# Optimization experiments

Hardware: AMD Instinct MI355X
Metric: run time of the kernel (lower is better)

Reference implementation:

```python
import jax, jax.numpy as jnp
import numpy as np

B, S, D, H = 2, 2048, 1024, 16  # batch, seq, embed_dim, num_heads
DH = D // H                      # head dim = 64


def setup_inputs() -> dict:
    key = jax.random.key(0)
    kx, kq, kbq, kk, kbk, kv, kbv = jax.random.split(key, 7)
    scale = 1.0 / np.sqrt(D)
    return {
        "x": jax.random.normal(kx, (B, S, D), dtype=jnp.float32),
        "Wq": jax.random.normal(kq, (D, D), dtype=jnp.float32) * scale,
        "bq": jax.random.normal(kbq, (D,), dtype=jnp.float32) * 0.01,
        "Wk": jax.random.normal(kk, (D, D), dtype=jnp.float32) * scale,
        "bk": jax.random.normal(kbk, (D,), dtype=jnp.float32) * 0.01,
        "Wv": jax.random.normal(kv, (D, D), dtype=jnp.float32) * scale,
        "bv": jax.random.normal(kbv, (D,), dtype=jnp.float32) * 0.01,
    }


def reference(x, Wq, bq, Wk, bk, Wv, bv):
    # ooqkv_type == 'q', odeint_method == 'id': q branch = act(Linear(x)), exact GELU (torch nn.GELU default)
    q = jax.nn.gelu(x @ Wq + bq, approximate=False)
    k = x @ Wk + bk
    v = x @ Wv + bv
    # [B, S, D] -> [B, S, H, DH]
    q = q.reshape(B, S, H, DH)
    k = k.reshape(B, S, H, DH)
    v = v.reshape(B, S, H, DH)
    # NOTE: original module has NO 1/sqrt(d) scale — faithful reproduction
    att = jnp.einsum("bqhd,bkhd->bhqk", q, k)
    att = jax.nn.softmax(att, axis=-1)
    out = jnp.einsum("bhqk,bkhd->bqhd", att, v)
    return out.reshape(B, S, D)
```

## Files before the change

### kernel.cpp

```cpp
#include <hip/hip_runtime.h>
#include <math.h>

#define B_  2
#define S_  2048
#define D_  1024
#define H_  16
#define DH_ 64
#define M_  (B_ * S_)

typedef _Float16 half_t;
typedef __attribute__((ext_vector_type(8))) _Float16 h8;
typedef __attribute__((ext_vector_type(4))) _Float16 h4;
typedef __attribute__((ext_vector_type(4))) float   f32x4;

__device__ __forceinline__ void gll16(const half_t* g, half_t* l) {
    __builtin_amdgcn_global_load_lds(
        (__attribute__((address_space(1))) const void*)g,
        (__attribute__((address_space(3))) void*)l, 16, 0, 0);
}

__global__ __launch_bounds__(256) void convert_x_k(
    const float* __restrict__ x, half_t* __restrict__ xh)
{
    const size_t i = ((size_t)blockIdx.x * 256 + threadIdx.x) * 8;
    const float4 a = *(const float4*)(x + i);
    const float4 b = *(const float4*)(x + i + 4);
    h8 o;
    o[0] = (half_t)a.x; o[1] = (half_t)a.y; o[2] = (half_t)a.z; o[3] = (half_t)a.w;
    o[4] = (half_t)b.x; o[5] = (half_t)b.y; o[6] = (half_t)b.z; o[7] = (half_t)b.w;
    *(h8*)(xh + i) = o;
}

__global__ __launch_bounds__(256) void transW_k(
    const float* __restrict__ Wq, const float* __restrict__ Wk,
    const float* __restrict__ Wv, half_t* __restrict__ Wt)
{
    const int which = blockIdx.y;
    const float* __restrict__ W = (which == 0) ? Wq : (which == 1) ? Wk : Wv;
    half_t* __restrict__ T = Wt + (size_t)which * D_ * D_;
    const int gw   = blockIdx.x * 4 + (threadIdx.x >> 6);
    const int lane = threadIdx.x & 63;
    const int n    = (gw & 15) * 64 + lane;
    const int k0   = (gw >> 4) * 8;
    h8 o;
    #pragma unroll
    for (int t = 0; t < 8; ++t) o[t] = (half_t)W[(size_t)(k0 + t) * D_ + n];
    *(h8*)(T + (size_t)n * D_ + k0) = o;
}

__global__ __launch_bounds__(256) void transV_k(
    const half_t* __restrict__ V, half_t* __restrict__ Vt)
{
    const int gw   = blockIdx.x * 4 + (threadIdx.x >> 6);
    const int lane = threadIdx.x & 63;
    const int bh   = gw >> 8;
    const int s0   = (gw & 255) * 8;
    const int b    = bh >> 4, h = bh & 15;
    h8 o;
    #pragma unroll
    for (int t = 0; t < 8; ++t)
        o[t] = V[((size_t)b * S_ + s0 + t) * D_ + h * DH_ + lane];
    *(h8*)(Vt + ((size_t)bh * DH_ + lane) * S_ + s0) = o;
}

__global__ __launch_bounds__(256) void qkv_gemm_f16(
    const half_t* __restrict__ xh, const half_t* __restrict__ Wt,
    const float* __restrict__ bq, const float* __restrict__ bk,
    const float* __restrict__ bv,
    half_t* __restrict__ Qo, half_t* __restrict__ Ko, half_t* __restrict__ Vo)
{
    const int n0g   = blockIdx.x * 128;
    const int which = n0g >> 10;
    const int n0    = n0g & 1023;
    const int m0    = blockIdx.y * 128;
    const half_t* __restrict__ Wp  = Wt + (size_t)which * D_ * D_;
    const float* __restrict__ bias = (which == 0) ? bq : (which == 1) ? bk : bv;
    half_t* __restrict__ out       = (which == 0) ? Qo : (which == 1) ? Ko : Vo;

    const int tid = threadIdx.x, lane = tid & 63, wave = tid >> 6;
    const int wm = (wave >> 1) * 64, wn = (wave & 1) * 64;
    const int ln = lane & 15, quad = lane >> 4;

    __shared__ __align__(16) half_t As[128][32];
    __shared__ __align__(16) half_t Bs[128][32];

    f32x4 acc[4][4];
    #pragma unroll
    for (int i = 0; i < 4; ++i)
        #pragma unroll
        for (int j = 0; j < 4; ++j) acc[i][j] = (f32x4){0.f, 0.f, 0.f, 0.f};

    for (int k0 = 0; k0 < D_; k0 += 32) {
        __syncthreads();
        #pragma unroll
        for (int l = 0; l < 2; ++l) {
            const int c = tid + l * 256;
            const int r = c >> 2, c8 = c & 3;
            gll16(xh + (size_t)(m0 + r) * D_ + k0 + c8 * 8, &As[r][c8 * 8]);
            gll16(Wp + (size_t)(n0 + r) * D_ + k0 + c8 * 8, &Bs[r][c8 * 8]);
        }
        __syncthreads();

        h8 af[4], bf[4];
        #pragma unroll
        for (int i = 0; i < 4; ++i) af[i] = *(const h8*)&As[wm + i * 16 + ln][quad * 8];
        #pragma unroll
        for (int j = 0; j < 4; ++j) bf[j] = *(const h8*)&Bs[wn + j * 16 + ln][quad * 8];
        #pragma unroll
        for (int i = 0; i < 4; ++i)
            #pragma unroll
            for (int j = 0; j < 4; ++j)
                acc[i][j] = __builtin_amdgcn_mfma_f32_16x16x32_f16(
                    af[i], bf[j], acc[i][j], 0, 0, 0);
    }

    #pragma unroll
    for (int j = 0; j < 4; ++j) {
        const int col = n0 + wn + j * 16 + ln;
        const float bb = bias[col];
        #pragma unroll
        for (int i = 0; i < 4; ++i) {
            #pragma unroll
            for (int r = 0; r < 4; ++r) {
                const int row = m0 + wm + i * 16 + quad * 4 + r;
                float t = acc[i][j][r] + bb;
                if (which == 0) t = 0.5f * t * (1.0f + erff(t * 0.70710678118654752f));
                out[(size_t)row * D_ + col] = (half_t)t;
            }
        }
    }
}

__global__ __launch_bounds__(256) void attn_f16(
    const half_t* __restrict__ Q, const half_t* __restrict__ K,
    const half_t* __restrict__ Vt, float* __restrict__ out)
{
    const int tid  = threadIdx.x;
    const int lane = tid & 63;
    const int wave = tid >> 6;
    const int ln   = lane & 15;
    const int quad = lane >> 4;
    const int bh   = blockIdx.y;
    const int b    = bh >> 4;
    const int h    = bh & 15;
    const int q0   = blockIdx.x * 64;

    const half_t* __restrict__ Qb  = Q  + (size_t)b * S_ * D_ + h * DH_;
    const half_t* __restrict__ Kb  = K  + (size_t)b * S_ * D_ + h * DH_;
    const half_t* __restrict__ Vtb = Vt + (size_t)bh * DH_ * S_;

    __shared__ __align__(16) half_t Ks[64][72];
    __shared__ __align__(16) half_t Vs[64][72];
    __shared__ __align__(16) half_t QPs[64][72];

    #pragma unroll
    for (int l = 0; l < 2; ++l) {
        const int c = tid + l * 256;
        const int r = c >> 3, k8 = c & 7;
        *(h8*)&QPs[r][k8 * 8] = *(const h8*)(Qb + (size_t)(q0 + r) * D_ + k8 * 8);
    }
    __syncthreads();
    const h8 qb0 = *(const h8*)&QPs[wave * 16 + ln][quad * 8];
    const h8 qb1 = *(const h8*)&QPs[wave * 16 + ln][32 + quad * 8];

    h8 ones8;
    #pragma unroll
    for (int t = 0; t < 8; ++t) ones8[t] = (half_t)1.0f;

    f32x4 O[4];
    #pragma unroll
    for (int j = 0; j < 4; ++j) O[j] = (f32x4){0.f, 0.f, 0.f, 0.f};
    f32x4 l5 = (f32x4){0.f, 0.f, 0.f, 0.f};
    float m_i = -INFINITY;

    for (int k0 = 0; k0 < S_; k0 += 64) {
        h8 kr[2], vr[2];
        #pragma unroll
        for (int l = 0; l < 2; ++l) {
            const int c = tid + l * 256;
            const int r = c >> 3, k8 = c & 7;
            kr[l] = *(const h8*)(Kb  + (size_t)(k0 + r) * D_ + k8 * 8);
            vr[l] = *(const h8*)(Vtb + (size_t)r * S_ + k0 + k8 * 8);
        }
        __syncthreads();
        #pragma unroll
        for (int l = 0; l < 2; ++l) {
            const int c = tid + l * 256;
            const int r = c >> 3, k8 = c & 7;
            *(h8*)&Ks[r][k8 * 8] = kr[l];
            *(h8*)&Vs[r][k8 * 8] = vr[l];
        }
        __syncthreads();

        f32x4 s[4];
        #pragma unroll
        for (int j = 0; j < 4; ++j) {
            const h8 ka0 = *(const h8*)&Ks[j * 16 + ln][quad * 8];
            const h8 ka1 = *(const h8*)&Ks[j * 16 + ln][32 + quad * 8];
            f32x4 t = (f32x4){0.f, 0.f, 0.f, 0.f};
            t = __builtin_amdgcn_mfma_f32_16x16x32_f16(ka0, qb0, t, 0, 0, 0);
            t = __builtin_amdgcn_mfma_f32_16x16x32_f16(ka1, qb1, t, 0, 0, 0);
            s[j] = t;
        }

        float mx = s[0][0];
        #pragma unroll
        for (int j = 0; j < 4; ++j)
            #pragma unroll
            for (int r = 0; r < 4; ++r) mx = fmaxf(mx, s[j][r]);
        mx = fmaxf(mx, __shfl_xor(mx, 16, 64));
        mx = fmaxf(mx, __shfl_xor(mx, 32, 64));
        const float mnew  = fmaxf(m_i, mx);
        const float alpha = __expf(m_i - mnew);
        m_i = mnew;

        #pragma unroll
        for (int j = 0; j < 4; ++j) {
            h4 pv;
            #pragma unroll
            for (int r = 0; r < 4; ++r) pv[r] = (half_t)__expf(s[j][r] - mnew);
            *(h4*)&QPs[wave * 16 + ln][j * 16 + quad * 4] = pv;
        }

        float ar[4];
        #pragma unroll
        for (int r = 0; r < 4; ++r) ar[r] = __shfl(alpha, quad * 4 + r, 64);
        #pragma unroll
        for (int r = 0; r < 4; ++r) {
            l5[r] *= ar[r];
            #pragma unroll
            for (int j = 0; j < 4; ++j) O[j][r] *= ar[r];
        }

        const h8 pa0 = *(const h8*)&QPs[wave * 16 + ln][quad * 8];
        const h8 pa1 = *(const h8*)&QPs[wave * 16 + ln][32 + quad * 8];
        #pragma unroll
        for (int j = 0; j < 4; ++j) {
            const h8 vb0 = *(const h8*)&Vs[j * 16 + ln][quad * 8];
            const h8 vb1 = *(const h8*)&Vs[j * 16 + ln][32 + quad * 8];
            O[j] = __builtin_amdgcn_mfma_f32_16x16x32_f16(pa0, vb0, O[j], 0, 0, 0);
            O[j] = __builtin_amdgcn_mfma_f32_16x16x32_f16(pa1, vb1, O[j], 0, 0, 0);
        }
        l5 = __builtin_amdgcn_mfma_f32_16x16x32_f16(pa0, ones8, l5, 0, 0, 0);
        l5 = __builtin_amdgcn_mfma_f32_16x16x32_f16(pa1, ones8, l5, 0, 0, 0);
    }

    #pragma unroll
    for (int r = 0; r < 4; ++r) {
        const float inv = 1.0f / l5[r];
        const int row = q0 + wave * 16 + quad * 4 + r;
        #pragma unroll
        for (int j = 0; j < 4; ++j)
            out[((size_t)b * S_ + row) * D_ + h * DH_ + j * 16 + ln] = O[j][r] * inv;
    }
}

extern "C" void kernel_launch(void* const* d_in, const int* in_sizes, int n_in,
                              void* d_out, int out_size, void* d_ws, size_t ws_size,
                              hipStream_t stream) {
    const float* x  = (const float*)d_in[0];
    const float* Wq = (const float*)d_in[1];
    const float* bq = (const float*)d_in[2];
    const float* Wk = (const float*)d_in[3];
    const float* bk = (const float*)d_in[4];
    const float* Wv = (const float*)d_in[5];
    const float* bv = (const float*)d_in[6];
    float* out = (float*)d_out;

    const size_t nmd = (size_t)M_ * D_;
    const size_t ndd = (size_t)D_ * D_;
    half_t* xh  = (half_t*)d_ws;
    half_t* Wt  = xh + nmd;
    half_t* Qh  = Wt + 3 * ndd;
    half_t* Kh  = Qh + nmd;
    half_t* Vh  = Kh + nmd;
    half_t* Vtw = Vh + nmd;

    convert_x_k<<<nmd / (256 * 8), 256, 0, stream>>>(x, xh);
    transW_k<<<dim3(512, 3), 256, 0, stream>>>(Wq, Wk, Wv, Wt);
    qkv_gemm_f16<<<dim3(3 * D_ / 128, M_ / 128), 256, 0, stream>>>(
        xh, Wt, bq, bk, bv, Qh, Kh, Vh);
    transV_k<<<2048, 256, 0, stream>>>(Vh, Vtw);
    attn_f16<<<dim3(S_ / 64, B_ * H_), 256, 0, stream>>>(Qh, Kh, Vtw, out);
}
```

Measured before the change: 209.1 us.

## Async swizzled K/V LDS loads, exp2 softmax, tanh GELU, conditional rescale

K and V tiles are now copied straight into LDS with global_load_lds, using an XOR-swizzled unpadded layout, instead of a register round-trip into padded arrays. The Q projection switches from exact erf GELU to a tanh-form approximation built on exp2 and rcp, and folds log2(e) into Q so softmax can use exp2. The online-softmax rescale of O and l is skipped when no row max grows in the wave. The trade-offs are GELU accuracy and losing the old overlap of next-tile register loads with the barrier, since loads are issued only after the sync.

New measurement: 197.9 us. 5.4% less time.

```diff
diff --git a/kernel.cpp b/kernel.cpp
--- a/kernel.cpp
+++ b/kernel.cpp
@@ -12,6 +12,8 @@
 typedef __attribute__((ext_vector_type(8))) _Float16 h8;
 typedef __attribute__((ext_vector_type(4))) _Float16 h4;
 typedef __attribute__((ext_vector_type(4))) float   f32x4;
+
+#define LOG2E 1.44269504088896f
 
 __device__ __forceinline__ void gll16(const half_t* g, half_t* l) {
     __builtin_amdgcn_global_load_lds(
@@ -124,7 +126,11 @@
             for (int r = 0; r < 4; ++r) {
                 const int row = m0 + wm + i * 16 + quad * 4 + r;
                 float t = acc[i][j][r] + bb;
-                if (which == 0) t = 0.5f * t * (1.0f + erff(t * 0.70710678118654752f));
+                if (which == 0) {
+                    const float u = t * fmaf(t * t, 0.0356774081f, 0.7978845608f);
+                    const float e = __builtin_amdgcn_exp2f(u * -2.88539008178f);
+                    t = t * __builtin_amdgcn_rcpf(1.0f + e) * LOG2E;
+                }
                 out[(size_t)row * D_ + col] = (half_t)t;
             }
         }
@@ -149,8 +155,8 @@
     const half_t* __restrict__ Kb  = K  + (size_t)b * S_ * D_ + h * DH_;
     const half_t* __restrict__ Vtb = Vt + (size_t)bh * DH_ * S_;
 
-    __shared__ __align__(16) half_t Ks[64][72];
-    __shared__ __align__(16) half_t Vs[64][72];
+    __shared__ __align__(16) half_t Ks[64 * 64];
+    __shared__ __align__(16) half_t Vs[64 * 64];
     __shared__ __align__(16) half_t QPs[64][72];
 
     #pragma unroll
@@ -174,70 +180,67 @@
     float m_i = -INFINITY;
 
     for (int k0 = 0; k0 < S_; k0 += 64) {
-        h8 kr[2], vr[2];
+        __syncthreads();
         #pragma unroll
         for (int l = 0; l < 2; ++l) {
             const int c = tid + l * 256;
-            const int r = c >> 3, k8 = c & 7;
-            kr[l] = *(const h8*)(Kb  + (size_t)(k0 + r) * D_ + k8 * 8);
-            vr[l] = *(const h8*)(Vtb + (size_t)r * S_ + k0 + k8 * 8);
-        }
-        __syncthreads();
-        #pragma unroll
-        for (int l = 0; l < 2; ++l) {
-            const int c = tid + l * 256;
-            const int r = c >> 3, k8 = c & 7;
-            *(h8*)&Ks[r][k8 * 8] = kr[l];
-            *(h8*)&Vs[r][k8 * 8] = vr[l];
+            const int r = c >> 3, c0 = c & 7;
+            const int cs = c0 ^ (r & 7);
+            gll16(Kb  + (size_t)(k0 + r) * D_ + cs * 8, &Ks[c * 8]);
+            gll16(Vtb + (size_t)r * S_ + k0 + cs * 8,   &Vs[c * 8]);
         }
         __syncthreads();
 
         f32x4 s[4];
         #pragma unroll
         for (int j = 0; j < 4; ++j) {
-            const h8 ka0 = *(const h8*)&Ks[j * 16 + ln][quad * 8];
-            const h8 ka1 = *(const h8*)&Ks[j * 16 + ln][32 + quad * 8];
+            const int rK = j * 16 + ln;
+            const h8 ka0 = *(const h8*)&Ks[rK * 64 + ((quad)     ^ (rK & 7)) * 8];
+            const h8 ka1 = *(const h8*)&Ks[rK * 64 + ((quad + 4) ^ (rK & 7)) * 8];
             f32x4 t = (f32x4){0.f, 0.f, 0.f, 0.f};
             t = __builtin_amdgcn_mfma_f32_16x16x32_f16(ka0, qb0, t, 0, 0, 0);
             t = __builtin_amdgcn_mfma_f32_16x16x32_f16(ka1, qb1, t, 0, 0, 0);
             s[j] = t;
         }
 
-        float mx = s[0][0];
-        #pragma unroll
-        for (int j = 0; j < 4; ++j)
-            #pragma unroll
-            for (int r = 0; r < 4; ++r) mx = fmaxf(mx, s[j][r]);
+        float mx = fmaxf(fmaxf(fmaxf(s[0][0], s[0][1]), fmaxf(s[0][2], s[0][3])),
+                         fmaxf(fmaxf(s[1][0], s[1][1]), fmaxf(s[1][2], s[1][3])));
+        mx = fmaxf(mx, fmaxf(fmaxf(fmaxf(s[2][0], s[2][1]), fmaxf(s[2][2], s[2][3])),
+                             fmaxf(fmaxf(s[3][0], s[3][1]), fmaxf(s[3][2], s[3][3]))));
         mx = fmaxf(mx, __shfl_xor(mx, 16, 64));
         mx = fmaxf(mx, __shfl_xor(mx, 32, 64));
-        const float mnew  = fmaxf(m_i, mx);
-        const float alpha = __expf(m_i - mnew);
-        m_i = mnew;
+
+        if (__ballot(mx > m_i)) {
+            const float mnew  = fmaxf(m_i, mx);
+            const float alpha = __builtin_amdgcn_exp2f(m_i - mnew);
+            m_i = mnew;
+            float ar[4];
+            #pragma unroll
+            for (int r = 0; r < 4; ++r) ar[r] = __shfl(alpha, quad * 4 + r, 64);
+            #pragma unroll
+            for (int r = 0; r < 4; ++r) {
+                l5[r] *= ar[r];
+                #pragma unroll
+                for (int j = 0; j < 4; ++j) O[j][r] *= ar[r];
+            }
+        }
 
         #pragma unroll
         for (int j = 0; j < 4; ++j) {
             h4 pv;
             #pragma unroll
-            for (int r = 0; r < 4; ++r) pv[r] = (half_t)__expf(s[j][r] - mnew);
+            for (int r = 0; r < 4; ++r)
+                pv[r] = (half_t)__builtin_amdgcn_exp2f(s[j][r] - m_i);
             *(h4*)&QPs[wave * 16 + ln][j * 16 + quad * 4] = pv;
-        }
-
-        float ar[4];
-        #pragma unroll
-        for (int r = 0; r < 4; ++r) ar[r] = __shfl(alpha, quad * 4 + r, 64);
-        #pragma unroll
-        for (int r = 0; r < 4; ++r) {
-            l5[r] *= ar[r];
-            #pragma unroll
-            for (int j = 0; j < 4; ++j) O[j][r] *= ar[r];
         }
 
         const h8 pa0 = *(const h8*)&QPs[wave * 16 + ln][quad * 8];
         const h8 pa1 = *(const h8*)&QPs[wave * 16 + ln][32 + quad * 8];
         #pragma unroll
         for (int j = 0; j < 4; ++j) {
-            const h8 vb0 = *(const h8*)&Vs[j * 16 + ln][quad * 8];
-            const h8 vb1 = *(const h8*)&Vs[j * 16 + ln][32 + quad * 8];
+            const int rV = j * 16 + ln;
+            const h8 vb0 = *(const h8*)&Vs[rV * 64 + ((quad)     ^ (rV & 7)) * 8];
+            const h8 vb1 = *(const h8*)&Vs[rV * 64 + ((quad + 4) ^ (rV & 7)) * 8];
             O[j] = __builtin_amdgcn_mfma_f32_16x16x32_f16(pa0, vb0, O[j], 0, 0, 0);
             O[j] = __builtin_amdgcn_mfma_f32_16x16x32_f16(pa1, vb1, O[j], 0, 0, 0);
         }
```
